# Performance work log

Hardware: AMD Instinct MI355X
Metric: run time of the kernel (lower is better)

Reference implementation:

```python
import jax, jax.numpy as jnp
import numpy as np

BN_EPS = 1e-5


def _conv1x1(w, x):
    # w: [out, in], x: [B, in, N] -> [B, out, N]
    return jnp.einsum('oi,bin->bon', w, x)


def _bn_eval(x, g, b, m, v):
    # x: [B, C, N]; eval-mode BatchNorm1d with running stats
    scale = (g / jnp.sqrt(v + BN_EPS))[None, :, None]
    shift = (b - m * g / jnp.sqrt(v + BN_EPS))[None, :, None]
    return x * scale + shift


def _sa_layer(x, xyz, wqk, wv, bvv, wt, btt, g, b2, m, v):
    # offset-attention (SALayerCLS). q_conv and k_conv share weights -> q == k.
    h = x + xyz                                   # [B, C, N]
    q = _conv1x1(wqk, h)                          # [B, C//4, N]
    val = _conv1x1(wv, h) + bvv[None, :, None]    # [B, C, N]
    energy = jnp.einsum('bdn,bdm->bnm', q, q)     # [B, N, N]
    att = jax.nn.softmax(energy, axis=-1)
    # double normalization: L1-renormalize over dim=1 (rows)
    att = att / (1e-9 + att.sum(axis=1, keepdims=True))
    x_r = jnp.einsum('bcn,bnm->bcm', val, att)    # [B, C, N]
    t = _conv1x1(wt, x - x_r) + btt[None, :, None]
    t = jax.nn.relu(_bn_eval(t, g, b2, m, v))
    return x + t


def setup_inputs() -> dict:
    key = jax.random.key(0)
    ks = jax.random.split(key, 17)
    B, C, N = 8, 256, 2048
    f = jnp.float32
    return {
        'x': jax.random.normal(ks[0], (B, C, N), f),
        'xyz': jax.random.normal(ks[1], (B, N, 3), f),
        'conv1_w': jax.random.normal(ks[2], (C, C), f) * 0.05,
        'convpos_w': jax.random.normal(ks[3], (C, 3), f) * 0.05,
        'bn1_g': jax.random.uniform(ks[4], (C,), f, 0.5, 1.5),
        'bn1_b': jax.random.normal(ks[5], (C,), f) * 0.05,
        'bn1_m': jax.random.normal(ks[6], (C,), f) * 0.05,
        'bn1_v': jax.random.uniform(ks[7], (C,), f, 0.5, 1.5),
        'Wqk': jax.random.normal(ks[8], (4, C // 4, C), f) * 0.05,
        'Wv': jax.random.normal(ks[9], (4, C, C), f) * 0.05,
        'bv': jax.random.normal(ks[10], (4, C), f) * 0.05,
        'Wt': jax.random.normal(ks[11], (4, C, C), f) * 0.05,
        'bt': jax.random.normal(ks[12], (4, C), f) * 0.05,
        'bn_g': jax.random.uniform(ks[13], (4, C), f, 0.5, 1.5),
        'bn_b': jax.random.normal(ks[14], (4, C), f) * 0.05,
        'bn_m': jax.random.normal(ks[15], (4, C), f) * 0.05,
        'bn_v': jax.random.uniform(ks[16], (4, C), f, 0.5, 1.5),
    }


def reference(x, xyz, conv1_w, convpos_w, bn1_g, bn1_b, bn1_m, bn1_v,
              Wqk, Wv, bv, Wt, bt, bn_g, bn_b, bn_m, bn_v):
    # xyz: [B, N, 3] -> conv_pos -> [B, C, N]
    pos = jnp.einsum('oi,bni->bon', convpos_w, xyz)
    h = jax.nn.relu(_bn_eval(_conv1x1(conv1_w, x), bn1_g, bn1_b, bn1_m, bn1_v))
    outs = []
    for i in range(4):  # four stacked SA layers (structurally distinct params)
        h = _sa_layer(h, pos, Wqk[i], Wv[i], bv[i], Wt[i], bt[i],
                      bn_g[i], bn_b[i], bn_m[i], bn_v[i])
        outs.append(h)
    return jnp.concatenate(outs, axis=1)  # [B, 4*C, N]
```

## Files before the change

kernel.cpp:

```cpp
#include <hip/hip_runtime.h>
#include <hip/hip_bf16.h>
#include <math.h>

#define B_DIM 8
#define C_DIM 256
#define N_DIM 2048
#define CQ 64

#define TM 64
#define TN 64
#define TK 16

#define NT 32

using short8 = __attribute__((ext_vector_type(8))) short;
using f32x4 = __attribute__((ext_vector_type(4))) float;

__device__ __forceinline__ unsigned short f2bf(float x) {
  union { float f; unsigned int u; } c; c.f = x;
  unsigned int r = c.u + 0x7fffu + ((c.u >> 16) & 1u);
  return (unsigned short)(r >> 16);
}
__device__ __forceinline__ float bf2f(unsigned short u) {
  union { unsigned int ui; float f; } c; c.ui = ((unsigned int)u) << 16;
  return c.f;
}

__global__ void split_kernel(const float* __restrict__ src, unsigned short* __restrict__ hi,
                             unsigned short* __restrict__ lo, int count) {
  int i = blockIdx.x * 256 + threadIdx.x;
  if (i < count) {
    float v = src[i];
    unsigned short h = f2bf(v);
    hi[i] = h;
    lo[i] = f2bf(v - bf2f(h));
  }
}

__global__ void pos_kernel(const float* __restrict__ w, const float* __restrict__ xyz,
                           float* __restrict__ pos) {
  int n = blockIdx.x * blockDim.x + threadIdx.x;
  int c = blockIdx.y;
  int b = blockIdx.z;
  const float* xp = xyz + ((long long)b * N_DIM + n) * 3;
  pos[((long long)b * C_DIM + c) * N_DIM + n] =
      w[c * 3 + 0] * xp[0] + w[c * 3 + 1] * xp[1] + w[c * 3 + 2] * xp[2];
}

__global__ void gemm_wx(const float* __restrict__ W,
                        const float* __restrict__ X, long long sxB,
                        const float* __restrict__ Xadd, long long saB,
                        const float* __restrict__ bias,
                        const float* __restrict__ bng, const float* __restrict__ bnb,
                        const float* __restrict__ bnm, const float* __restrict__ bnv,
                        const float* __restrict__ Res, long long srB,
                        float* __restrict__ Y, unsigned short* __restrict__ Ybf,
                        long long syB, int M, int K) {
  const int N = N_DIM;
  int b = blockIdx.z;
  int m0 = blockIdx.y * TM;
  int n0 = blockIdx.x * TN;
  int t = threadIdx.x;
  int tx = t & 15, ty = t >> 4;
  __shared__ float As[TK][TM + 1];
  __shared__ float Bs[TK][TN];
  float acc[4][4] = {};
  const float* Xb = X + (long long)b * sxB;
  const float* Ab = Xadd ? Xadd + (long long)b * saB : nullptr;
  for (int k0 = 0; k0 < K; k0 += TK) {
#pragma unroll
    for (int v = 0; v < 4; v++) {
      int l = t * 4 + v;
      int i = l >> 4, k = l & 15;
      As[k][i] = W[(long long)(m0 + i) * K + k0 + k];
    }
#pragma unroll
    for (int v = 0; v < 4; v++) {
      int l = t * 4 + v;
      int k = l >> 6, j = l & 63;
      float x = Xb[(long long)(k0 + k) * N + n0 + j];
      if (Ab) x += Ab[(long long)(k0 + k) * N + n0 + j];
      Bs[k][j] = x;
    }
    __syncthreads();
#pragma unroll
    for (int k = 0; k < TK; k++) {
      float a[4], bb[4];
#pragma unroll
      for (int ii = 0; ii < 4; ii++) a[ii] = As[k][ty * 4 + ii];
#pragma unroll
      for (int jj = 0; jj < 4; jj++) bb[jj] = Bs[k][tx * 4 + jj];
#pragma unroll
      for (int ii = 0; ii < 4; ii++)
#pragma unroll
        for (int jj = 0; jj < 4; jj++)
          acc[ii][jj] = fmaf(a[ii], bb[jj], acc[ii][jj]);
    }
    __syncthreads();
  }
#pragma unroll
  for (int ii = 0; ii < 4; ii++) {
    int m = m0 + ty * 4 + ii;
    float sh = bias ? bias[m] : 0.f;
    bool dobn = (bng != nullptr);
    float bnsc = 0.f, bnsh = 0.f;
    if (dobn) {
      bnsc = bng[m] * rsqrtf(bnv[m] + 1e-5f);
      bnsh = bnb[m] - bnm[m] * bnsc;
    }
#pragma unroll
    for (int jj = 0; jj < 4; jj++) {
      int n = n0 + tx * 4 + jj;
      float v = acc[ii][jj] + sh;
      if (dobn) v = fmaxf(v * bnsc + bnsh, 0.f);
      if (Res) v += Res[(long long)b * srB + (long long)m * N + n];
      if (Ybf)
        Ybf[(long long)b * syB + (long long)m * N + n] = f2bf(v);
      else
        Y[(long long)b * syB + (long long)m * N + n] = v;
    }
  }
}

template <bool XLO>
__global__ __launch_bounds__(256) void gemm_mfma(
    const unsigned short* __restrict__ Whi, const unsigned short* __restrict__ Wlo,
    const float* __restrict__ X, long long sxB,
    const float* __restrict__ Xadd, long long saB,
    const float* __restrict__ bias,
    const float* __restrict__ bng, const float* __restrict__ bnb,
    const float* __restrict__ bnm, const float* __restrict__ bnv,
    const float* __restrict__ Res, long long srB,
    float* __restrict__ Y, unsigned short* __restrict__ Ybf, long long syB) {
  const int N = N_DIM, K = C_DIM;
  int b = blockIdx.z;
  int m0 = blockIdx.y * 128;
  int n0 = blockIdx.x * 64;
  int t = threadIdx.x;
  int w = t >> 6, l = t & 63;
  int lr = l & 15, lk = l >> 4;
  int j = t & 63, dq = t >> 6;
  int ar = t >> 3, as_ = t & 7;

  __shared__ __align__(16) char Ah[128 * 128];
  __shared__ __align__(16) char Al[128 * 128];
  __shared__ __align__(16) char Bh[64 * 128];
  __shared__ __align__(16) char Bl[XLO ? 64 * 128 : 16];

  const float* Xb = X + (long long)b * sxB;
  const float* Adb = Xadd ? Xadd + (long long)b * saB : nullptr;

  f32x4 acc[2][4];
#pragma unroll
  for (int i = 0; i < 2; i++)
#pragma unroll
    for (int jq = 0; jq < 4; jq++) acc[i][jq] = f32x4{0.f, 0.f, 0.f, 0.f};

  for (int k0 = 0; k0 < K; k0 += 64) {
    short8 wh[4], wl[4];
#pragma unroll
    for (int it = 0; it < 4; it++) {
      int r = it * 32 + ar;
      wh[it] = *(const short8*)(Whi + (long long)(m0 + r) * K + k0 + as_ * 8);
      wl[it] = *(const short8*)(Wlo + (long long)(m0 + r) * K + k0 + as_ * 8);
    }
    float v[16];
#pragma unroll
    for (int i = 0; i < 16; i++) {
      float x = Xb[(long long)(k0 + dq * 16 + i) * N + n0 + j];
      if (Adb) x += Adb[(long long)(k0 + dq * 16 + i) * N + n0 + j];
      v[i] = x;
    }
    unsigned int ph[8], pl[8];
#pragma unroll
    for (int i = 0; i < 8; i++) {
      unsigned short h0 = f2bf(v[2 * i]), h1 = f2bf(v[2 * i + 1]);
      ph[i] = (unsigned int)h0 | ((unsigned int)h1 << 16);
      if (XLO) {
        unsigned short l0 = f2bf(v[2 * i] - bf2f(h0)), l1 = f2bf(v[2 * i + 1] - bf2f(h1));
        pl[i] = (unsigned int)l0 | ((unsigned int)l1 << 16);
      }
    }
#pragma unroll
    for (int it = 0; it < 4; it++) {
      int r = it * 32 + ar;
      *(short8*)(Ah + r * 128 + ((as_ ^ (r & 7)) << 4)) = wh[it];
      *(short8*)(Al + r * 128 + ((as_ ^ (r & 7)) << 4)) = wl[it];
    }
    {
      int o0 = dq * 2, o1 = dq * 2 + 1;
      *(uint4*)(Bh + j * 128 + ((o0 ^ (j & 7)) << 4)) = make_uint4(ph[0], ph[1], ph[2], ph[3]);
      *(uint4*)(Bh + j * 128 + ((o1 ^ (j & 7)) << 4)) = make_uint4(ph[4], ph[5], ph[6], ph[7]);
      if (XLO) {
        *(uint4*)(Bl + j * 128 + ((o0 ^ (j & 7)) << 4)) = make_uint4(pl[0], pl[1], pl[2], pl[3]);
        *(uint4*)(Bl + j * 128 + ((o1 ^ (j & 7)) << 4)) = make_uint4(pl[4], pl[5], pl[6], pl[7]);
      }
    }
    __syncthreads();
#pragma unroll
    for (int sub = 0; sub < 2; sub++) {
      short8 ah[2], al2[2], bh[4], bl[4];
#pragma unroll
      for (int mi = 0; mi < 2; mi++) {
        int ra = w * 32 + mi * 16 + lr;
        ah[mi] = *(const short8*)(Ah + ra * 128 + (((sub * 4 + lk) ^ (ra & 7)) << 4));
        al2[mi] = *(const short8*)(Al + ra * 128 + (((sub * 4 + lk) ^ (ra & 7)) << 4));
      }
#pragma unroll
      for (int ni = 0; ni < 4; ni++) {
        int rb = ni * 16 + lr;
        bh[ni] = *(const short8*)(Bh + rb * 128 + (((sub * 4 + lk) ^ (rb & 7)) << 4));
        if (XLO) bl[ni] = *(const short8*)(Bl + rb * 128 + (((sub * 4 + lk) ^ (rb & 7)) << 4));
      }
#pragma unroll
      for (int mi = 0; mi < 2; mi++)
#pragma unroll
        for (int ni = 0; ni < 4; ni++) {
          acc[mi][ni] = __builtin_amdgcn_mfma_f32_16x16x32_bf16(ah[mi], bh[ni], acc[mi][ni], 0, 0, 0);
          if (XLO)
            acc[mi][ni] = __builtin_amdgcn_mfma_f32_16x16x32_bf16(ah[mi], bl[ni], acc[mi][ni], 0, 0, 0);
          acc[mi][ni] = __builtin_amdgcn_mfma_f32_16x16x32_bf16(al2[mi], bh[ni], acc[mi][ni], 0, 0, 0);
        }
    }
    __syncthreads();
  }
#pragma unroll
  for (int mi = 0; mi < 2; mi++) {
#pragma unroll
    for (int jj = 0; jj < 4; jj++) {
      int m = m0 + w * 32 + mi * 16 + lk * 4 + jj;
      float sh = bias ? bias[m] : 0.f;
      bool dobn = (bng != nullptr);
      float bnsc = 0.f, bnsh = 0.f;
      if (dobn) {
        bnsc = bng[m] * rsqrtf(bnv[m] + 1e-5f);
        bnsh = bnb[m] - bnm[m] * bnsc;
      }
#pragma unroll
      for (int ni = 0; ni < 4; ni++) {
        int n = n0 + ni * 16 + lr;
        float vv = acc[mi][ni][jj] + sh;
        if (dobn) vv = fmaxf(vv * bnsc + bnsh, 0.f);
        if (Res) vv += Res[(long long)b * srB + (long long)m * N + n];
        if (Ybf)
          Ybf[(long long)b * syB + (long long)m * N + n] = f2bf(vv);
        else
          Y[(long long)b * syB + (long long)m * N + n] = vv;
      }
    }
  }
}

__global__ __launch_bounds__(256) void energy_mfma(const float* __restrict__ q,
                                                   float* __restrict__ E,
                                                   float2* __restrict__ Epart) {
  const int N = N_DIM;
  int b = blockIdx.z;
  int r0 = blockIdx.y * 64;
  int cp = blockIdx.x;
  int t = threadIdx.x;
  int w = t >> 6, l = t & 63;
  int lr = l & 15, lk = l >> 4;
  int j = t & 63, dq = t >> 6;

  __shared__ __align__(16) char Ah[64 * 128];
  __shared__ __align__(16) char Al[64 * 128];
  __shared__ __align__(16) char Bh[64 * 128];
  __shared__ __align__(16) char Bl[64 * 128];

  const float* qb = q + (long long)b * CQ * N;
  {
    float va[16];
#pragma unroll
    for (int i = 0; i < 16; i++) va[i] = qb[(long long)(dq * 16 + i) * N + r0 + j];
    unsigned int pah[8], pal[8];
#pragma unroll
    for (int i = 0; i < 8; i++) {
      unsigned short h0 = f2bf(va[2 * i]), h1 = f2bf(va[2 * i + 1]);
      unsigned short l0 = f2bf(va[2 * i] - bf2f(h0)), l1 = f2bf(va[2 * i + 1] - bf2f(h1));
      pah[i] = (unsigned int)h0 | ((unsigned int)h1 << 16);
      pal[i] = (unsigned int)l0 | ((unsigned int)l1 << 16);
    }
    int o0 = dq * 2, o1 = dq * 2 + 1;
    *(uint4*)(Ah + j * 128 + ((o0 ^ (j & 7)) << 4)) = make_uint4(pah[0], pah[1], pah[2], pah[3]);
    *(uint4*)(Ah + j * 128 + ((o1 ^ (j & 7)) << 4)) = make_uint4(pah[4], pah[5], pah[6], pah[7]);
    *(uint4*)(Al + j * 128 + ((o0 ^ (j & 7)) << 4)) = make_uint4(pal[0], pal[1], pal[2], pal[3]);
    *(uint4*)(Al + j * 128 + ((o1 ^ (j & 7)) << 4)) = make_uint4(pal[4], pal[5], pal[6], pal[7]);
  }

  float mrun[4], srun[4];
#pragma unroll
  for (int jj = 0; jj < 4; jj++) { mrun[jj] = -3.0e38f; srun[jj] = 0.f; }

  for (int ct = 0; ct < 2; ct++) {
    int c0 = cp * 128 + ct * 64;
    float vb_[16];
#pragma unroll
    for (int i = 0; i < 16; i++) vb_[i] = qb[(long long)(dq * 16 + i) * N + c0 + j];
    unsigned int pbh[8], pbl[8];
#pragma unroll
    for (int i = 0; i < 8; i++) {
      unsigned short g0 = f2bf(vb_[2 * i]), g1 = f2bf(vb_[2 * i + 1]);
      unsigned short m0_ = f2bf(vb_[2 * i] - bf2f(g0)), m1 = f2bf(vb_[2 * i + 1] - bf2f(g1));
      pbh[i] = (unsigned int)g0 | ((unsigned int)g1 << 16);
      pbl[i] = (unsigned int)m0_ | ((unsigned int)m1 << 16);
    }
    __syncthreads();
    {
      int o0 = dq * 2, o1 = dq * 2 + 1;
      *(uint4*)(Bh + j * 128 + ((o0 ^ (j & 7)) << 4)) = make_uint4(pbh[0], pbh[1], pbh[2], pbh[3]);
      *(uint4*)(Bh + j * 128 + ((o1 ^ (j & 7)) << 4)) = make_uint4(pbh[4], pbh[5], pbh[6], pbh[7]);
      *(uint4*)(Bl + j * 128 + ((o0 ^ (j & 7)) << 4)) = make_uint4(pbl[0], pbl[1], pbl[2], pbl[3]);
      *(uint4*)(Bl + j * 128 + ((o1 ^ (j & 7)) << 4)) = make_uint4(pbl[4], pbl[5], pbl[6], pbl[7]);
    }
    __syncthreads();

    f32x4 acc[4];
#pragma unroll
    for (int i = 0; i < 4; i++) acc[i] = f32x4{0.f, 0.f, 0.f, 0.f};
#pragma unroll
    for (int sub = 0; sub < 2; sub++) {
      int ra = w * 16 + lr;
      short8 ah = *(const short8*)(Ah + ra * 128 + (((sub * 4 + lk) ^ (ra & 7)) << 4));
      short8 al = *(const short8*)(Al + ra * 128 + (((sub * 4 + lk) ^ (ra & 7)) << 4));
      short8 bh[4], bl[4];
#pragma unroll
      for (int ni = 0; ni < 4; ni++) {
        int rb = ni * 16 + lr;
        bh[ni] = *(const short8*)(Bh + rb * 128 + (((sub * 4 + lk) ^ (rb & 7)) << 4));
        bl[ni] = *(const short8*)(Bl + rb * 128 + (((sub * 4 + lk) ^ (rb & 7)) << 4));
      }
#pragma unroll
      for (int ni = 0; ni < 4; ni++) {
        acc[ni] = __builtin_amdgcn_mfma_f32_16x16x32_bf16(ah, bh[ni], acc[ni], 0, 0, 0);
        acc[ni] = __builtin_amdgcn_mfma_f32_16x16x32_bf16(ah, bl[ni], acc[ni], 0, 0, 0);
        acc[ni] = __builtin_amdgcn_mfma_f32_16x16x32_bf16(al, bh[ni], acc[ni], 0, 0, 0);
      }
    }
    long long base = (long long)b * N * N;
#pragma unroll
    for (int ni = 0; ni < 4; ni++)
#pragma unroll
      for (int jj = 0; jj < 4; jj++)
        E[base + (long long)(r0 + w * 16 + lk * 4 + jj) * N + c0 + ni * 16 + lr] = acc[ni][jj];

#pragma unroll
    for (int jj = 0; jj < 4; jj++) {
      float vmax = fmaxf(fmaxf(acc[0][jj], acc[1][jj]), fmaxf(acc[2][jj], acc[3][jj]));
#pragma unroll
      for (int msk = 1; msk < 16; msk <<= 1) vmax = fmaxf(vmax, __shfl_xor(vmax, msk, 64));
      float ssum = 0.f;
#pragma unroll
      for (int ni = 0; ni < 4; ni++) ssum += __expf(acc[ni][jj] - vmax);
#pragma unroll
      for (int msk = 1; msk < 16; msk <<= 1) ssum += __shfl_xor(ssum, msk, 64);
      float Mn = fmaxf(mrun[jj], vmax);
      srun[jj] = srun[jj] * __expf(mrun[jj] - Mn) + ssum * __expf(vmax - Mn);
      mrun[jj] = Mn;
    }
  }
  const long long BNr = (long long)B_DIM * N_DIM;
  if (lr == 0) {
#pragma unroll
    for (int jj = 0; jj < 4; jj++) {
      long long row = (long long)b * N + r0 + w * 16 + lk * 4 + jj;
      Epart[(long long)cp * BNr + row] = make_float2(mrun[jj], srun[jj]);
    }
  }
}

__global__ void rowstats2(const float2* __restrict__ Epart, float* __restrict__ rmax,
                          float* __restrict__ rinv) {
  const long long BNr = (long long)B_DIM * N_DIM;
  int rloc = threadIdx.x & 63, qd = threadIdx.x >> 6;
  long long row = (long long)blockIdx.x * 64 + rloc;
  float2 v[4];
  float m = -3.4e38f;
#pragma unroll
  for (int i = 0; i < 4; i++) {
    v[i] = Epart[(long long)(qd * 4 + i) * BNr + row];
    m = fmaxf(m, v[i].x);
  }
  float s = 0.f;
#pragma unroll
  for (int i = 0; i < 4; i++) s += v[i].y * __expf(v[i].x - m);
  __shared__ float sm[4][64], ss[4][64];
  sm[qd][rloc] = m;
  ss[qd][rloc] = s;
  __syncthreads();
  if (qd == 0) {
    float M = fmaxf(fmaxf(sm[0][rloc], sm[1][rloc]), fmaxf(sm[2][rloc], sm[3][rloc]));
    float S = ss[0][rloc] * __expf(sm[0][rloc] - M) + ss[1][rloc] * __expf(sm[1][rloc] - M) +
              ss[2][rloc] * __expf(sm[2][rloc] - M) + ss[3][rloc] * __expf(sm[3][rloc] - M);
    rmax[row] = M;
    rinv[row] = 1.0f / S;
  }
}

__global__ __launch_bounds__(512, 4) void pv_mfma(
    const unsigned short* __restrict__ valbf,
    const float* __restrict__ E,
    const float* __restrict__ rmax, const float* __restrict__ rinv,
    const float* __restrict__ Hprev, long long shB, float* __restrict__ D) {
  const int N = N_DIM;
  int b = blockIdx.z;
  int n0 = blockIdx.x * NT;
  int t = threadIdx.x;
  int w = t >> 6, l = t & 63;
  int lr = l & 15, lk = l >> 4;
  int brow = t >> 4, kq = t & 15;

  __shared__ __align__(16) char As[C_DIM * 128];
  __shared__ __align__(16) char Bs[NT * 128];
  __shared__ float csfin[NT];

  const unsigned short* vb = valbf + (long long)b * C_DIM * N;
  const float* Ebr = E + ((long long)b * N + n0 + brow) * N;
  const float* rm = rmax + (long long)b * N;
  const float* ri = rinv + (long long)b * N;

  f32x4 acc[2][2];
#pragma unroll
  for (int i = 0; i < 2; i++)
#pragma unroll
    for (int jq = 0; jq < 2; jq++) acc[i][jq] = f32x4{0.f, 0.f, 0.f, 0.f};
  float cs = 0.f;

  const int kl = kq * 4;
  float4 ev = *(const float4*)(Ebr + kl);
  float4 rv = *(const float4*)(rm + kl);
  float4 iv = *(const float4*)(ri + kl);
  short8 areg[4];
#pragma unroll
  for (int it = 0; it < 4; it++) {
    int idx = it * 512 + t;
    int r = idx >> 3, s = idx & 7;
    areg[it] = *(const short8*)(vb + (long long)r * N + s * 8);
  }

  for (int k0 = 0; k0 < N; k0 += 64) {
    __syncthreads();
    {
      float a0 = __expf(ev.x - rv.x) * iv.x;
      float a1 = __expf(ev.y - rv.y) * iv.y;
      float a2 = __expf(ev.z - rv.z) * iv.z;
      float a3 = __expf(ev.w - rv.w) * iv.w;
      unsigned short u0 = f2bf(a0), u1 = f2bf(a1), u2 = f2bf(a2), u3 = f2bf(a3);
      cs += bf2f(u0) + bf2f(u1) + bf2f(u2) + bf2f(u3);
      uint2 pk;
      pk.x = (unsigned int)u0 | ((unsigned int)u1 << 16);
      pk.y = (unsigned int)u2 | ((unsigned int)u3 << 16);
      *(uint2*)(Bs + brow * 128 + ((((kl >> 3) ^ (brow & 7)) << 4) | ((kl & 7) * 2))) = pk;
    }
#pragma unroll
    for (int it = 0; it < 4; it++) {
      int idx = it * 512 + t;
      int r = idx >> 3, s = idx & 7;
      *(short8*)(As + r * 128 + ((s ^ (r & 7)) << 4)) = areg[it];
    }
    __syncthreads();
    if (k0 + 64 < N) {
      int kb = k0 + 64;
      ev = *(const float4*)(Ebr + kb + kl);
      rv = *(const float4*)(rm + kb + kl);
      iv = *(const float4*)(ri + kb + kl);
#pragma unroll
      for (int it = 0; it < 4; it++) {
        int idx = it * 512 + t;
        int r = idx >> 3, s = idx & 7;
        areg[it] = *(const short8*)(vb + (long long)r * N + kb + s * 8);
      }
    }
#pragma unroll
    for (int sub = 0; sub < 2; sub++) {
      short8 bq[2];
#pragma unroll
      for (int ni = 0; ni < 2; ni++) {
        int rn = ni * 16 + lr;
        bq[ni] = *(const short8*)(Bs + rn * 128 + (((sub * 4 + lk) ^ (rn & 7)) << 4));
      }
#pragma unroll
      for (int mi = 0; mi < 2; mi++) {
        int ra = w * 32 + mi * 16 + lr;
        short8 af = *(const short8*)(As + ra * 128 + (((sub * 4 + lk) ^ (ra & 7)) << 4));
#pragma unroll
        for (int ni = 0; ni < 2; ni++)
          acc[mi][ni] = __builtin_amdgcn_mfma_f32_16x16x32_bf16(af, bq[ni], acc[mi][ni], 0, 0, 0);
      }
    }
  }

  cs += __shfl_xor(cs, 1, 64);
  cs += __shfl_xor(cs, 2, 64);
  cs += __shfl_xor(cs, 4, 64);
  cs += __shfl_xor(cs, 8, 64);
  if (kq == 0) csfin[brow] = 1.0f / (1e-9f + cs);
  __syncthreads();

  const float* Hb = Hprev + (long long)b * shB;
  float* Db = D + (long long)b * C_DIM * N;
#pragma unroll
  for (int mi = 0; mi < 2; mi++) {
#pragma unroll
    for (int ni = 0; ni < 2; ni++) {
#pragma unroll
      for (int jj = 0; jj < 4; jj++) {
        int cr = w * 32 + mi * 16 + lk * 4 + jj;
        int ml = ni * 16 + lr;
        float xr = acc[mi][ni][jj] * csfin[ml];
        Db[(long long)cr * N + n0 + ml] = Hb[(long long)cr * N + n0 + ml] - xr;
      }
    }
  }
}

extern "C" void kernel_launch(void* const* d_in, const int* in_sizes, int n_in,
                              void* d_out, int out_size, void* d_ws, size_t ws_size,
                              hipStream_t stream) {
  const float* x = (const float*)d_in[0];
  const float* xyz = (const float*)d_in[1];
  const float* conv1_w = (const float*)d_in[2];
  const float* convpos_w = (const float*)d_in[3];
  const float* bn1_g = (const float*)d_in[4];
  const float* bn1_b = (const float*)d_in[5];
  const float* bn1_m = (const float*)d_in[6];
  const float* bn1_v = (const float*)d_in[7];
  const float* Wqk = (const float*)d_in[8];
  const float* Wv = (const float*)d_in[9];
  const float* bv = (const float*)d_in[10];
  const float* Wt = (const float*)d_in[11];
  const float* bt = (const float*)d_in[12];
  const float* bng = (const float*)d_in[13];
  const float* bnb = (const float*)d_in[14];
  const float* bnm = (const float*)d_in[15];
  const float* bnv = (const float*)d_in[16];
  float* out = (float*)d_out;

  const long long BCN = (long long)B_DIM * C_DIM * N_DIM;
  const long long CN = (long long)C_DIM * N_DIM;
  const long long BN = (long long)B_DIM * N_DIM;
  const int WSZ = C_DIM * C_DIM;
  float* ws = (float*)d_ws;
  float* pos = ws;
  float* h0 = pos + BCN;
  float* qbuf = h0 + BCN;
  float* dbuf = qbuf + (long long)B_DIM * CQ * N_DIM;
  float* rmax = dbuf + BCN;
  float* rinv = rmax + BN;
  unsigned short* valbf = (unsigned short*)(rinv + BN);
  unsigned short* whi = valbf + BCN;
  unsigned short* wlo = whi + 9 * WSZ;
  float2* Epart = (float2*)(wlo + 9 * WSZ);
  float* E = (float*)(Epart + 32 * BN);

  unsigned short* c1hi = whi;
  unsigned short* c1lo = wlo;
  unsigned short* wvhi = whi + WSZ;
  unsigned short* wvlo = wlo + WSZ;
  unsigned short* wthi = whi + 5 * WSZ;
  unsigned short* wtlo = wlo + 5 * WSZ;

  dim3 blk(256);

  split_kernel<<<dim3(WSZ / 256), blk, 0, stream>>>(conv1_w, c1hi, c1lo, WSZ);
  split_kernel<<<dim3(4 * WSZ / 256), blk, 0, stream>>>(Wv, wvhi, wvlo, 4 * WSZ);
  split_kernel<<<dim3(4 * WSZ / 256), blk, 0, stream>>>(Wt, wthi, wtlo, 4 * WSZ);

  pos_kernel<<<dim3(N_DIM / 256, C_DIM, B_DIM), blk, 0, stream>>>(convpos_w, xyz, pos);

  gemm_mfma<true><<<dim3(N_DIM / 64, 2, B_DIM), blk, 0, stream>>>(
      c1hi, c1lo, x, CN, nullptr, 0, nullptr,
      bn1_g, bn1_b, bn1_m, bn1_v, nullptr, 0, h0, nullptr, CN);

  for (int i = 0; i < 4; i++) {
    const float* hp = (i == 0) ? h0 : out + (long long)(i - 1) * CN;
    long long shp = (i == 0) ? CN : 4 * CN;

    gemm_wx<<<dim3(N_DIM / TN, CQ / TM, B_DIM), blk, 0, stream>>>(
        Wqk + (long long)i * CQ * C_DIM, hp, shp, pos, CN, nullptr,
        nullptr, nullptr, nullptr, nullptr, nullptr, 0,
        qbuf, nullptr, (long long)CQ * N_DIM, CQ, C_DIM);

    gemm_mfma<false><<<dim3(N_DIM / 64, 2, B_DIM), blk, 0, stream>>>(
        wvhi + (long long)i * WSZ, wvlo + (long long)i * WSZ, hp, shp, pos, CN,
        bv + i * C_DIM, nullptr, nullptr, nullptr, nullptr, nullptr, 0,
        nullptr, valbf, CN);

    energy_mfma<<<dim3(N_DIM / 128, N_DIM / 64, B_DIM), blk, 0, stream>>>(qbuf, E, Epart);

    rowstats2<<<dim3(B_DIM * N_DIM / 64), blk, 0, stream>>>(Epart, rmax, rinv);

    pv_mfma<<<dim3(N_DIM / NT, 1, B_DIM), dim3(512), 0, stream>>>(
        valbf, E, rmax, rinv, hp, shp, dbuf);

    gemm_mfma<true><<<dim3(N_DIM / 64, 2, B_DIM), blk, 0, stream>>>(
        wthi + (long long)i * WSZ, wtlo + (long long)i * WSZ, dbuf, CN, nullptr, 0,
        bt + i * C_DIM, bng + i * C_DIM, bnb + i * C_DIM, bnm + i * C_DIM,
        bnv + i * C_DIM, hp, shp, out + (long long)i * CN, nullptr, 4 * CN);
  }
}
```

Before: 814.9 us.

## Store energy matrix as fp16 and double-buffer LDS in PV kernel

```diff
diff --git a/kernel.cpp b/kernel.cpp
--- a/kernel.cpp
+++ b/kernel.cpp
@@ -24,6 +24,16 @@
 __device__ __forceinline__ float bf2f(unsigned short u) {
   union { unsigned int ui; float f; } c; c.ui = ((unsigned int)u) << 16;
   return c.f;
+}
+__device__ __forceinline__ unsigned short f2h(float x) {
+  union { _Float16 h; unsigned short u; } c;
+  c.h = (_Float16)x;
+  return c.u;
+}
+__device__ __forceinline__ float h2f(unsigned short u) {
+  union { _Float16 h; unsigned short u; } c;
+  c.u = u;
+  return (float)c.h;
 }
 
 __global__ void split_kernel(const float* __restrict__ src, unsigned short* __restrict__ hi,
@@ -252,7 +262,7 @@
 }
 
 __global__ __launch_bounds__(256) void energy_mfma(const float* __restrict__ q,
-                                                   float* __restrict__ E,
+                                                   unsigned short* __restrict__ Eh,
                                                    float2* __restrict__ Epart) {
   const int N = N_DIM;
   int b = blockIdx.z;
@@ -342,7 +352,8 @@
     for (int ni = 0; ni < 4; ni++)
 #pragma unroll
       for (int jj = 0; jj < 4; jj++)
-        E[base + (long long)(r0 + w * 16 + lk * 4 + jj) * N + c0 + ni * 16 + lr] = acc[ni][jj];
+        Eh[base + (long long)(r0 + w * 16 + lk * 4 + jj) * N + c0 + ni * 16 + lr] =
+            f2h(acc[ni][jj]);
 
 #pragma unroll
     for (int jj = 0; jj < 4; jj++) {
@@ -397,9 +408,59 @@
   }
 }
 
+#define PV_LOAD(kb)                                                            \
+  {                                                                            \
+    ev = *(const ushort4*)(Ehr + (kb) + kl);                                   \
+    rv = *(const float4*)(rm + (kb) + kl);                                     \
+    iv = *(const float4*)(ri + (kb) + kl);                                     \
+    _Pragma("unroll") for (int it = 0; it < 4; it++) {                         \
+      int idx = it * 512 + t;                                                  \
+      int r = idx >> 3, s = idx & 7;                                           \
+      areg[it] = *(const short8*)(vb + (long long)r * N + (kb) + s * 8);       \
+    }                                                                          \
+  }
+
+#define PV_STAGE(bu)                                                           \
+  {                                                                            \
+    float a0 = __expf(h2f(ev.x) - rv.x) * iv.x;                                \
+    float a1 = __expf(h2f(ev.y) - rv.y) * iv.y;                                \
+    float a2 = __expf(h2f(ev.z) - rv.z) * iv.z;                                \
+    float a3 = __expf(h2f(ev.w) - rv.w) * iv.w;                                \
+    unsigned short u0 = f2bf(a0), u1 = f2bf(a1), u2 = f2bf(a2), u3 = f2bf(a3); \
+    cs += bf2f(u0) + bf2f(u1) + bf2f(u2) + bf2f(u3);                           \
+    uint2 pk;                                                                  \
+    pk.x = (unsigned int)u0 | ((unsigned int)u1 << 16);                        \
+    pk.y = (unsigned int)u2 | ((unsigned int)u3 << 16);                        \
+    *(uint2*)(Bs[bu] + brow * 128 +                                            \
+              ((((kl >> 3) ^ (brow & 7)) << 4) | ((kl & 7) * 2))) = pk;        \
+    _Pragma("unroll") for (int it = 0; it < 4; it++) {                         \
+      int idx = it * 512 + t;                                                  \
+      int r = idx >> 3, s = idx & 7;                                           \
+      *(short8*)(As[bu] + r * 128 + ((s ^ (r & 7)) << 4)) = areg[it];          \
+    }                                                                          \
+  }
+
+#define PV_COMPUTE(bu)                                                         \
+  _Pragma("unroll") for (int sub = 0; sub < 2; sub++) {                        \
+    short8 bq[2];                                                              \
+    _Pragma("unroll") for (int ni = 0; ni < 2; ni++) {                         \
+      int rn = ni * 16 + lr;                                                   \
+      bq[ni] = *(const short8*)(Bs[bu] + rn * 128 +                            \
+                                (((sub * 4 + lk) ^ (rn & 7)) << 4));           \
+    }                                                                          \
+    _Pragma("unroll") for (int mi = 0; mi < 2; mi++) {                         \
+      int ra = w * 32 + mi * 16 + lr;                                          \
+      short8 af = *(const short8*)(As[bu] + ra * 128 +                         \
+                                   (((sub * 4 + lk) ^ (ra & 7)) << 4));        \
+      _Pragma("unroll") for (int ni = 0; ni < 2; ni++)                         \
+          acc[mi][ni] = __builtin_amdgcn_mfma_f32_16x16x32_bf16(               \
+              af, bq[ni], acc[mi][ni], 0, 0, 0);                               \
+    }                                                                          \
+  }
+
 __global__ __launch_bounds__(512, 4) void pv_mfma(
     const unsigned short* __restrict__ valbf,
-    const float* __restrict__ E,
+    const unsigned short* __restrict__ Eh,
     const float* __restrict__ rmax, const float* __restrict__ rinv,
     const float* __restrict__ Hprev, long long shB, float* __restrict__ D) {
   const int N = N_DIM;
@@ -410,12 +471,12 @@
   int lr = l & 15, lk = l >> 4;
   int brow = t >> 4, kq = t & 15;
 
-  __shared__ __align__(16) char As[C_DIM * 128];
-  __shared__ __align__(16) char Bs[NT * 128];
+  __shared__ __align__(16) char As[2][C_DIM * 128];
+  __shared__ __align__(16) char Bs[2][NT * 128];
   __shared__ float csfin[NT];
 
   const unsigned short* vb = valbf + (long long)b * C_DIM * N;
-  const float* Ebr = E + ((long long)b * N + n0 + brow) * N;
+  const unsigned short* Ehr = Eh + ((long long)b * N + n0 + brow) * N;
   const float* rm = rmax + (long long)b * N;
   const float* ri = rinv + (long long)b * N;
 
@@ -425,69 +486,26 @@
 #pragma unroll
     for (int jq = 0; jq < 2; jq++) acc[i][jq] = f32x4{0.f, 0.f, 0.f, 0.f};
   float cs = 0.f;
-
   const int kl = kq * 4;
-  float4 ev = *(const float4*)(Ebr + kl);
-  float4 rv = *(const float4*)(rm + kl);
-  float4 iv = *(const float4*)(ri + kl);
+
+  ushort4 ev;
+  float4 rv, iv;
   short8 areg[4];
-#pragma unroll
-  for (int it = 0; it < 4; it++) {
-    int idx = it * 512 + t;
-    int r = idx >> 3, s = idx & 7;
-    areg[it] = *(const short8*)(vb + (long long)r * N + s * 8);
-  }
-
-  for (int k0 = 0; k0 < N; k0 += 64) {
+
+  PV_LOAD(0);
+  PV_STAGE(0);
+  PV_LOAD(64);
+  __syncthreads();
+
+  const int NTILES = N / 64;
+  for (int i = 0; i < NTILES; i++) {
+    int cur = i & 1;
+    PV_COMPUTE(cur);
+    if (i < NTILES - 1) {
+      PV_STAGE(cur ^ 1);
+      if (i < NTILES - 2) PV_LOAD((i + 2) * 64);
+    }
     __syncthreads();
-    {
-      float a0 = __expf(ev.x - rv.x) * iv.x;
-      float a1 = __expf(ev.y - rv.y) * iv.y;
-      float a2 = __expf(ev.z - rv.z) * iv.z;
-      float a3 = __expf(ev.w - rv.w) * iv.w;
-      unsigned short u0 = f2bf(a0), u1 = f2bf(a1), u2 = f2bf(a2), u3 = f2bf(a3);
-      cs += bf2f(u0) + bf2f(u1) + bf2f(u2) + bf2f(u3);
-      uint2 pk;
-      pk.x = (unsigned int)u0 | ((unsigned int)u1 << 16);
-      pk.y = (unsigned int)u2 | ((unsigned int)u3 << 16);
-      *(uint2*)(Bs + brow * 128 + ((((kl >> 3) ^ (brow & 7)) << 4) | ((kl & 7) * 2))) = pk;
-    }
-#pragma unroll
-    for (int it = 0; it < 4; it++) {
-      int idx = it * 512 + t;
-      int r = idx >> 3, s = idx & 7;
-      *(short8*)(As + r * 128 + ((s ^ (r & 7)) << 4)) = areg[it];
-    }
-    __syncthreads();
-    if (k0 + 64 < N) {
-      int kb = k0 + 64;
-      ev = *(const float4*)(Ebr + kb + kl);
-      rv = *(const float4*)(rm + kb + kl);
-      iv = *(const float4*)(ri + kb + kl);
-#pragma unroll
-      for (int it = 0; it < 4; it++) {
-        int idx = it * 512 + t;
-        int r = idx >> 3, s = idx & 7;
-        areg[it] = *(const short8*)(vb + (long long)r * N + kb + s * 8);
-      }
-    }
-#pragma unroll
-    for (int sub = 0; sub < 2; sub++) {
-      short8 bq[2];
-#pragma unroll
-      for (int ni = 0; ni < 2; ni++) {
-        int rn = ni * 16 + lr;
-        bq[ni] = *(const short8*)(Bs + rn * 128 + (((sub * 4 + lk) ^ (rn & 7)) << 4));
-      }
-#pragma unroll
-      for (int mi = 0; mi < 2; mi++) {
-        int ra = w * 32 + mi * 16 + lr;
-        short8 af = *(const short8*)(As + ra * 128 + (((sub * 4 + lk) ^ (ra & 7)) << 4));
-#pragma unroll
-        for (int ni = 0; ni < 2; ni++)
-          acc[mi][ni] = __builtin_amdgcn_mfma_f32_16x16x32_bf16(af, bq[ni], acc[mi][ni], 0, 0, 0);
-      }
-    }
   }
 
   cs += __shfl_xor(cs, 1, 64);
@@ -551,7 +569,7 @@
   unsigned short* whi = valbf + BCN;
   unsigned short* wlo = whi + 9 * WSZ;
   float2* Epart = (float2*)(wlo + 9 * WSZ);
-  float* E = (float*)(Epart + 32 * BN);
+  unsigned short* Eh = (unsigned short*)(Epart + 32 * BN);
 
   unsigned short* c1hi = whi;
   unsigned short* c1lo = wlo;
@@ -586,12 +604,12 @@
         bv + i * C_DIM, nullptr, nullptr, nullptr, nullptr, nullptr, 0,
         nullptr, valbf, CN);
 
-    energy_mfma<<<dim3(N_DIM / 128, N_DIM / 64, B_DIM), blk, 0, stream>>>(qbuf, E, Epart);
+    energy_mfma<<<dim3(N_DIM / 128, N_DIM / 64, B_DIM), blk, 0, stream>>>(qbuf, Eh, Epart);
 
     rowstats2<<<dim3(B_DIM * N_DIM / 64), blk, 0, stream>>>(Epart, rmax, rinv);
 
     pv_mfma<<<dim3(N_DIM / NT, 1, B_DIM), dim3(512), 0, stream>>>(
-        valbf, E, rmax, rinv, hp, shp, dbuf);
+        valbf, Eh, rmax, rinv, hp, shp, dbuf);
 
     gemm_mfma<true><<<dim3(N_DIM / 64, 2, B_DIM), blk, 0, stream>>>(
         wthi + (long long)i * WSZ, wtlo + (long long)i * WSZ, dbuf, CN, nullptr, 0,
```

New measurement: 781.7 us. 4.1% less time.
